# Optimization experiments

Measured on AMD Instinct MI355X. Metric: run time of the kernel, lower is better.

The kernel has to match this reference:

```python
import jax, jax.numpy as jnp
import numpy as np

B, C, H, W = 4, 64, 160, 160
OUT = 64
KS = (5, 7)


def conv2d(x, w, b=None, pad=0, groups=1):
    y = jax.lax.conv_general_dilated(
        x, w, (1, 1), [(pad, pad), (pad, pad)],
        feature_group_count=groups,
        dimension_numbers=('NCHW', 'OIHW', 'NCHW'))
    return y if b is None else y + b[None, :, None, None]


def bn_eval(x, g, b, m, v, eps=1e-5):
    s = g / jnp.sqrt(v + eps)
    return x * s[None, :, None, None] + (b - m * s)[None, :, None, None]


def boundary_attn(x, w1, b1, w2, b2):
    Cc = x.shape[1]
    kx = jnp.array([[-1., 0., 1.], [-2., 0., 2.], [-1., 0., 1.]], jnp.float32)
    ky = jnp.array([[-1., -2., -1.], [0., 0., 0.], [1., 2., 1.]], jnp.float32)
    sobel = jnp.concatenate([jnp.tile(kx[None, None], (Cc, 1, 1, 1)),
                             jnp.tile(ky[None, None], (Cc, 1, 1, 1))], axis=0)  # [2C,1,3,3]
    # grouped conv (groups=C): same output-channel grouping semantics as torch
    edge = jnp.abs(conv2d(x, sobel, pad=1, groups=Cc))
    edge = (edge[:, :Cc] + edge[:, Cc:]).mean(axis=1, keepdims=True)
    a = jax.nn.relu(conv2d(x, w1, b1, pad=1))
    a = conv2d(a, w2, b2, pad=0)
    a = jax.nn.sigmoid(a + edge)
    return x * a + x


def icc(off, half_k):
    # iterative cumulative constraint over the (small, static) K channel axis
    K = off.shape[1]
    cs = [None] * K
    cs[half_k] = off[:, half_k]
    for i in range(1, half_k + 1):
        cs[half_k - i] = 0.5 * cs[half_k - i + 1] + 0.5 * off[:, half_k - i]
        cs[half_k + i] = 0.5 * cs[half_k + i - 1] + 0.5 * off[:, half_k + i]
    c = jnp.stack(cs, axis=1)
    w = jnp.ones((K, 1, 3, 3), jnp.float32) / 9.0
    return conv2d(c, w, pad=1, groups=K)


def tumor_center(x):
    _, _, Hx, Wx = x.shape
    fs = x.mean(axis=1)  # [B,H,W]
    hg = jnp.arange(Hx, dtype=x.dtype)[None, :, None]
    wg = jnp.arange(Wx, dtype=x.dtype)[None, None, :]
    tot = fs.sum(axis=(1, 2)) + 1e-6
    return (fs * hg).sum(axis=(1, 2)) / tot, (fs * wg).sum(axis=(1, 2)) / tot


def dyn1d(x, kw, kb, K, O):
    # Original Dynamic1DConv reshapes x to [B*H*W, C, 1, 1] and grid_samples a
    # [1,K] grid per pixel. With align_corners=True a 1x1 input maps every grid
    # coordinate to ix=iy=0, so sampled[n,c,k] == x[b,c,h,w] for all k; the
    # bmm with per-pixel kernels followed by sum over C therefore collapses to
    # (sum_c x) * (sum_k kernels) -- same math, no giant gather materialized.
    Bx, _, Hx, Wx = x.shape
    ker = conv2d(x, kw, kb, pad=0).reshape(Bx, O, K, Hx, Wx)
    return x.sum(axis=1, keepdims=True) * ker.sum(axis=2)


def reference(x, ba_w1, ba_b1, ba_w2, ba_b2,
              off_w1, off_b1, off_bn_g, off_bn_b, off_bn_m, off_bn_v,
              off_w2, off_b2,
              rk5_w, rk5_b, rk7_w, rk7_b,
              lk5_w, lk5_b, lk7_w, lk7_b,
              sf_w, sf_b, sf_bn_g, sf_bn_b, sf_bn_m, sf_bn_v,
              fc_w, fc_b):
    residual = x  # in_channels == out_channels -> nn.Identity
    xa = boundary_attn(x, ba_w1, ba_b1, ba_w2, ba_b2)
    # offset branch (faithful to original; mathematically dead because the
    # per-pixel grid_sample ignores its grid -- see dyn1d). BN in eval mode.
    raw = conv2d(xa, off_w1, off_b1, pad=1)
    raw = jax.nn.relu(bn_eval(raw, off_bn_g, off_bn_b, off_bn_m, off_bn_v))
    raw = conv2d(raw, off_w2, off_b2, pad=1)
    sumk, idx = sum(KS), 0
    _offs = []
    for k in KS:
        _offs.append(icc(jnp.tanh(raw[:, idx:idx + k]), k // 2))
        _offs.append(icc(jnp.tanh(raw[:, sumk + idx:sumk + idx + k]), k // 2))
        idx += k
    _hc, _wc = tumor_center(xa)  # also dead w.r.t. output
    O = OUT // 2 // len(KS)  # 16 channels per scale per flow type
    feats = [dyn1d(xa, rk5_w, rk5_b, 5, O), dyn1d(xa, rk7_w, rk7_b, 7, O),
             dyn1d(xa, lk5_w, lk5_b, 5, O), dyn1d(xa, lk7_w, lk7_b, 7, O)]
    fusion = jnp.concatenate(feats, axis=1)  # [B, OUT, H, W]
    y = jax.nn.relu(bn_eval(conv2d(fusion, sf_w, sf_b, pad=1),
                            sf_bn_g, sf_bn_b, sf_bn_m, sf_bn_v))
    y = conv2d(y, fc_w, fc_b, pad=0)
    return y + residual


def setup_inputs() -> dict:
    key = jax.random.key(0)
    keys = iter(jax.random.split(key, 40))
    def nrm(shape, s=0.05):
        return jax.random.normal(next(keys), shape, jnp.float32) * s
    d = {}
    d['x'] = nrm((B, C, H, W), 1.0)
    d['ba_w1'] = nrm((C // 2, C, 3, 3)); d['ba_b1'] = nrm((C // 2,))
    d['ba_w2'] = nrm((1, C // 2, 1, 1)); d['ba_b2'] = nrm((1,))
    d['off_w1'] = nrm((C // 2, C, 3, 3)); d['off_b1'] = nrm((C // 2,))
    d['off_bn_g'] = 1.0 + nrm((C // 2,)); d['off_bn_b'] = nrm((C // 2,))
    d['off_bn_m'] = nrm((C // 2,))
    d['off_bn_v'] = jax.random.uniform(next(keys), (C // 2,), jnp.float32, 0.5, 1.5)
    d['off_w2'] = nrm((2 * sum(KS), C // 2, 3, 3)); d['off_b2'] = nrm((2 * sum(KS),))
    O = OUT // 2 // len(KS)
    for name, k in (('rk5', 5), ('rk7', 7), ('lk5', 5), ('lk7', 7)):
        d[name + '_w'] = nrm((O * k, C, 1, 1)); d[name + '_b'] = nrm((O * k,))
    d['sf_w'] = nrm((OUT, OUT, 3, 3)); d['sf_b'] = nrm((OUT,))
    d['sf_bn_g'] = 1.0 + nrm((OUT,)); d['sf_bn_b'] = nrm((OUT,))
    d['sf_bn_m'] = nrm((OUT,))
    d['sf_bn_v'] = jax.random.uniform(next(keys), (OUT,), jnp.float32, 0.5, 1.5)
    d['fc_w'] = nrm((OUT, OUT, 1, 1)); d['fc_b'] = nrm((OUT,))
    return d
```

## Files before the change

### kernel.cpp

```cpp
#include <hip/hip_runtime.h>
#include <hip/hip_bf16.h>
#include <math.h>

#define BB 4
#define CC 64
#define HH 160
#define WW 160
#define HWs (HH*WW)
#define NPIX (BB*HWs)

using bf16 = __hip_bfloat16;
typedef __attribute__((ext_vector_type(8)))  short short8v;
typedef __attribute__((ext_vector_type(16))) float float16v;

__device__ __forceinline__ unsigned short f2bfu(float f){
    union { bf16 h; unsigned short u; } cv; cv.h = __float2bfloat16(f); return cv.u;
}
__device__ __forceinline__ float bfu2f(unsigned short u){
    union { float f; unsigned int i; } cv; cv.i = ((unsigned int)u)<<16; return cv.f;
}
__device__ __forceinline__ float16v fzero16(){
    float16v z;
    #pragma unroll
    for(int i=0;i<16;i++) z[i]=0.f;
    return z;
}

constexpr int B1X1 = 0;
constexpr int SFBo = 64;
constexpr int SFWf = 128;
constexpr int BAWf = 18560;
constexpr int FUWf = 27776;
constexpr int FCWf = 29824;
constexpr int WS_FLOATS = 31872;

__global__ void k_prep(const float* __restrict__ rk5w, const float* __restrict__ rk5b,
                       const float* __restrict__ rk7w, const float* __restrict__ rk7b,
                       const float* __restrict__ lk5w, const float* __restrict__ lk5b,
                       const float* __restrict__ lk7w, const float* __restrict__ lk7b,
                       const float* __restrict__ sfw,  const float* __restrict__ sfb,
                       const float* __restrict__ bng,  const float* __restrict__ bnb,
                       const float* __restrict__ bnm,  const float* __restrict__ bnv,
                       const float* __restrict__ baw1, const float* __restrict__ fcw,
                       float* __restrict__ ws)
{
    int tid = blockIdx.x*blockDim.x + threadIdx.x;
    int nt  = gridDim.x*blockDim.x;
    for(int o=tid;o<64;o+=nt){
        int grp=o>>4, oo=o&15; int K=(grp&1)?7:5;
        const float* bp = (grp==0)?rk5b:(grp==1)?rk7b:(grp==2)?lk5b:lk7b;
        float s=0.f; for(int k=0;k<K;k++) s += bp[oo*K+k];
        ws[B1X1+o]=s;
    }
    for(int oc=tid;oc<64;oc+=nt){
        float sc = bng[oc]*rsqrtf(bnv[oc]+1e-5f);
        ws[SFBo+oc] = sfb[oc]*sc + bnb[oc] - bnm[oc]*sc;
    }
    unsigned short* sfwf = (unsigned short*)(ws + SFWf);
    for(int idx=tid; idx<36864; idx+=nt){
        int og = idx/18432;  int rem = idx - og*18432;
        int f  = rem>>9;     int r2 = rem & 511;
        int lane = r2>>3;    int j = r2&7;
        int tap = f>>2, kc = f&3;
        int oc = og*32 + (lane&31);
        int ic = kc*16 + (lane>>5)*8 + j;
        float sc = bng[oc]*rsqrtf(bnv[oc]+1e-5f);
        sfwf[idx] = f2bfu(sfw[(oc*64+ic)*9 + tap] * sc);
    }
    unsigned short* bawf = (unsigned short*)(ws + BAWf);
    for(int idx=tid; idx<18432; idx+=nt){
        int f  = idx>>9;     int r2 = idx & 511;
        int lane = r2>>3;    int j = r2&7;
        int tap = f>>2, kc = f&3;
        int oc = lane&31;
        int ic = kc*16 + (lane>>5)*8 + j;
        bawf[idx] = f2bfu(baw1[(oc*64+ic)*9 + tap]);
    }
    unsigned short* fuwf = (unsigned short*)(ws + FUWf);
    for(int idx=tid; idx<4096; idx+=nt){
        int og   = idx>>11;
        int kc   = (idx>>9)&3;
        int lane = (idx>>3)&63;
        int j    = idx&7;
        int oc = og*32 + (lane&31);
        int c  = kc*16 + (lane>>5)*8 + j;
        int grp = oc>>4, oo = oc&15; int K = (grp&1)?7:5;
        const float* w = (grp==0)?rk5w:(grp==1)?rk7w:(grp==2)?lk5w:lk7w;
        float s = 0.f;
        for(int k=0;k<K;k++) s += w[(oo*K+k)*64 + c];
        fuwf[idx] = f2bfu(s);
    }
    unsigned short* fcwf = (unsigned short*)(ws + FCWf);
    for(int idx=tid; idx<4096; idx+=nt){
        int og   = idx>>11;
        int kc   = (idx>>9)&3;
        int lane = (idx>>3)&63;
        int j    = idx&7;
        int oc = og*32 + (lane&31);
        int c  = kc*16 + (lane>>5)*8 + j;
        fcwf[idx] = f2bfu(fcw[oc*64 + c]);
    }
}

__global__ __launch_bounds__(256)
void k_x2nhwc(const float* __restrict__ x, unsigned short* __restrict__ xb)
{
    __shared__ unsigned short ls[128*72];
    const int t = threadIdx.x;
    const int p0 = blockIdx.x*128;
    const int b = p0 / HWs, pp0 = p0 % HWs;
    const float4* xb4 = (const float4*)(x + (size_t)b*CC*HWs + pp0);
    #pragma unroll
    for(int iter=0; iter<8; iter++){
        int idx = iter*256 + t;
        int c = idx>>5, g = idx&31;
        float4 v = xb4[(size_t)c*(HWs/4) + g];
        int px = g*4;
        int bs = (c>>3) ^ ((g>>1)&7);
        unsigned short* base = ls + bs*8 + (c&7);
        base[(px+0)*72] = f2bfu(v.x);
        base[(px+1)*72] = f2bfu(v.y);
        base[(px+2)*72] = f2bfu(v.z);
        base[(px+3)*72] = f2bfu(v.w);
    }
    __syncthreads();
    #pragma unroll
    for(int iter=0; iter<4; iter++){
        int idx = iter*256 + t;
        int sub = idx&7, px = idx>>3;
        int bs = sub ^ ((px>>3)&7);
        short8v v = *(short8v*)(ls + px*72 + bs*8);
        *(short8v*)(xb + ((size_t)(p0+px))*64 + sub*8) = v;
    }
}

__global__ __launch_bounds__(256)
void k_fuse(const unsigned short* __restrict__ xb, const float* __restrict__ bab1,
            const float* __restrict__ baw2, const float* __restrict__ bab2,
            const float* __restrict__ ws, const float* __restrict__ fcb,
            const float* __restrict__ x, float* __restrict__ out)
{
    __shared__ unsigned short xt[240*72];
    __shared__ unsigned short ftile[180*72];
    __shared__ float ebuf[2][180];
    const int bw = blockIdx.x, bh = blockIdx.y, b = blockIdx.z;
    const int t = threadIdx.x;
    const int wave = t>>6, lane = t&63;
    const int half = lane>>5, n = lane&31;
    const int w0 = bw*16, h0 = bh*8;

    const unsigned short* fb = xb + (size_t)b*HWs*64;
    for(int idx=t; idx<1920; idx+=256){
        int sub = idx&7; int pix = idx>>3;
        int r = pix/20, c = pix - r*20;
        int gh = h0-2+r, gw = w0-2+c;
        short8v v = {0,0,0,0,0,0,0,0};
        if(gh>=0&&gh<HH&&gw>=0&&gw<WW)
            v = *(const short8v*)(fb + ((size_t)(gh*WW+gw))*64 + sub*8);
        *(short8v*)(xt + pix*72 + sub*8) = v;
    }
    __syncthreads();

    float czr[2], sxr[2];
    const unsigned short* bawf = (const unsigned short*)(ws + BAWf);
    #pragma unroll
    for(int rep=0; rep<2; rep++){
        int g = wave + rep*4;
        if(g < 6){
            int p = g*32 + n; if(p > 179) p = 179;
            int pr = p/18, pc = p - pr*18;
            float16v acc = fzero16();
            #pragma unroll
            for(int kc=0; kc<4; kc++){
                short8v af[9];
                #pragma unroll
                for(int tap=0; tap<9; tap++)
                    af[tap] = *(const short8v*)(bawf + (((size_t)(tap*4+kc))*64 + lane)*8);
                #pragma unroll
                for(int tap=0; tap<9; tap++){
                    const int dh = tap/3, dw = tap%3;
                    short8v bf = *(const short8v*)(xt + ((pr+dh)*20 + pc+dw)*72
                                                   + kc*16 + half*8);
                    acc = __builtin_amdgcn_mfma_f32_32x32x16_bf16(af[tap], bf, acc, 0,0,0);
                }
            }
            float cz = 0.f;
            #pragma unroll
            for(int r=0;r<16;r++){
                int oc = (r&3) + 8*(r>>2) + 4*half;
                cz += fmaxf(acc[r]+bab1[oc],0.f)*baw2[oc];
            }
            cz += __shfl_xor(cz, 32);
            czr[rep] = cz;
            short8v ones;
            #pragma unroll
            for(int j=0;j<8;j++) ones[j] = (short)0x3F80;
            float16v s = fzero16();
            #pragma unroll
            for(int kc=0; kc<4; kc++){
                short8v bf = *(const short8v*)(xt + ((pr+1)*20 + pc+1)*72 + kc*16 + half*8);
                s = __builtin_amdgcn_mfma_f32_32x32x16_bf16(ones, bf, s, 0,0,0);
            }
            sxr[rep] = s[0];
        }
    }

    for(int idx=t; idx<360; idx+=256){
        const int hf = (idx>=180) ? 1 : 0;
        const int px2 = idx - hf*180;
        const int r = px2/18, c = px2 - (px2/18)*18;
        float e = 0.f;
        #pragma unroll
        for(int s=0; s<4; s++){
            const int sub = hf*4 + s;
            if(hf==0){
                short8v a0 = *(const short8v*)(xt + ((r  )*20 + c  )*72 + sub*8);
                short8v a2 = *(const short8v*)(xt + ((r  )*20 + c+2)*72 + sub*8);
                short8v a3 = *(const short8v*)(xt + ((r+1)*20 + c  )*72 + sub*8);
                short8v a5 = *(const short8v*)(xt + ((r+1)*20 + c+2)*72 + sub*8);
                short8v a6 = *(const short8v*)(xt + ((r+2)*20 + c  )*72 + sub*8);
                short8v a8 = *(const short8v*)(xt + ((r+2)*20 + c+2)*72 + sub*8);
                #pragma unroll
                for(int j=0;j<8;j++){
                    float gx = (bfu2f((unsigned short)a2[j]) - bfu2f((unsigned short)a0[j]))
                       + 2.f*(bfu2f((unsigned short)a5[j]) - bfu2f((unsigned short)a3[j]))
                       +      (bfu2f((unsigned short)a8[j]) - bfu2f((unsigned short)a6[j]));
                    e += fabsf(gx);
                }
            } else {
                short8v b0 = *(const short8v*)(xt + ((r  )*20 + c  )*72 + sub*8);
                short8v b1 = *(const short8v*)(xt + ((r  )*20 + c+1)*72 + sub*8);
                short8v b2 = *(const short8v*)(xt + ((r  )*20 + c+2)*72 + sub*8);
                short8v b6 = *(const short8v*)(xt + ((r+2)*20 + c  )*72 + sub*8);
                short8v b7 = *(const short8v*)(xt + ((r+2)*20 + c+1)*72 + sub*8);
                short8v b8 = *(const short8v*)(xt + ((r+2)*20 + c+2)*72 + sub*8);
                #pragma unroll
                for(int j=0;j<8;j++){
                    float gy = (bfu2f((unsigned short)b6[j]) - bfu2f((unsigned short)b0[j]))
                       + 2.f*(bfu2f((unsigned short)b7[j]) - bfu2f((unsigned short)b1[j]))
                       +      (bfu2f((unsigned short)b8[j]) - bfu2f((unsigned short)b2[j]));
                    e += fabsf(gy);
                }
            }
        }
        ebuf[hf][px2] = e;
    }
    __syncthreads();

    const unsigned short* fuwf = (const unsigned short*)(ws + FUWf);
    #pragma unroll
    for(int rep=0; rep<2; rep++){
        int g = wave + rep*4;
        if(g < 6){
            int p0g = g*32 + n;
            bool wr = (p0g < 180);
            int p = wr ? p0g : 179;
            int pr = p/18, pc = p - pr*18;
            float z = czr[rep] + bab2[0] + (ebuf[0][p] + ebuf[1][p]) * (1.f/32.f);
            float A = 1.f + 1.f/(1.f+__expf(-z));
            float Q = A * sxr[rep];
            float P = A * Q;
            #pragma unroll
            for(int og=0; og<2; og++){
                float16v a = fzero16();
                #pragma unroll
                for(int kc=0; kc<4; kc++){
                    short8v wf = *(const short8v*)(fuwf + (((size_t)og*4 + kc)*64 + lane)*8);
                    short8v bf = *(const short8v*)(xt + ((pr+1)*20 + pc+1)*72 + kc*16 + half*8);
                    a = __builtin_amdgcn_mfma_f32_32x32x16_bf16(wf, bf, a, 0,0,0);
                }
                float bq[16];
                #pragma unroll
                for(int r=0;r<16;r++) bq[r] = ws[B1X1 + og*32 + (r&3)+8*(r>>2)+4*half];
                unsigned short* base = ftile + p*72 + og*32 + 4*half;
                #pragma unroll
                for(int gq=0; gq<4; gq++){
                    union { unsigned long long u; unsigned short s[4]; } pk;
                    #pragma unroll
                    for(int rr=0; rr<4; rr++)
                        pk.s[rr] = f2bfu(P*a[4*gq+rr] + Q*bq[4*gq+rr]);
                    if(wr) *(unsigned long long*)(base + 8*gq) = pk.u;
                }
            }
        }
    }
    __syncthreads();

    const int row = 2*wave + (n>>4), col = n&15;
    const unsigned short* sfwf = (const unsigned short*)(ws + SFWf);
    const unsigned short* fcwf = (const unsigned short*)(ws + FCWf);
    float16v F0 = fzero16(), F1 = fzero16();

    #pragma unroll
    for(int og=0; og<2; og++){
        float16v Y = fzero16();
        #pragma unroll
        for(int kc=0; kc<4; kc++){
            short8v af[9];
            #pragma unroll
            for(int tap=0; tap<9; tap++)
                af[tap] = *(const short8v*)(sfwf + (((size_t)og*36 + tap*4+kc)*64 + lane)*8);
            #pragma unroll
            for(int tap=0; tap<9; tap++){
                const int dh = tap/3, dw = tap%3;
                short8v bf = *(const short8v*)(ftile + ((row+dh)*18 + col+dw)*72
                                               + kc*16 + half*8);
                Y = __builtin_amdgcn_mfma_f32_32x32x16_bf16(af[tap], bf, Y, 0,0,0);
            }
        }
        unsigned short yb[16];
        #pragma unroll
        for(int r=0;r<16;r++){
            float bias = ws[SFBo + og*32 + (r&3)+8*(r>>2)+4*half];
            yb[r] = f2bfu(fmaxf(Y[r] + bias, 0.f));
        }
        #pragma unroll
        for(int kcl=0; kcl<2; kcl++){
            const int kc_fc = 2*og + kcl;
            unsigned short l0,l1,l2,l3, s0,s1,s2,s3;
            if(half==0){ l0=yb[8*kcl+0]; l1=yb[8*kcl+1]; l2=yb[8*kcl+2]; l3=yb[8*kcl+3];
                         s0=yb[8*kcl+4]; s1=yb[8*kcl+5]; s2=yb[8*kcl+6]; s3=yb[8*kcl+7]; }
            else       { l0=yb[8*kcl+4]; l1=yb[8*kcl+5]; l2=yb[8*kcl+6]; l3=yb[8*kcl+7];
                         s0=yb[8*kcl+0]; s1=yb[8*kcl+1]; s2=yb[8*kcl+2]; s3=yb[8*kcl+3]; }
            int p0 = (int)((unsigned)s0 | ((unsigned)s1<<16));
            int p1 = (int)((unsigned)s2 | ((unsigned)s3<<16));
            int r0 = __shfl_xor(p0, 32);
            int r1 = __shfl_xor(p1, 32);
            unsigned short m0 = (unsigned short)(r0 & 0xffff);
            unsigned short m1 = (unsigned short)(((unsigned)r0) >> 16);
            unsigned short m2 = (unsigned short)(r1 & 0xffff);
            unsigned short m3 = (unsigned short)(((unsigned)r1) >> 16);
            short8v B;
            if(half==0){ B[0]=(short)l0; B[1]=(short)l1; B[2]=(short)l2; B[3]=(short)l3;
                         B[4]=(short)m0; B[5]=(short)m1; B[6]=(short)m2; B[7]=(short)m3; }
            else       { B[0]=(short)m0; B[1]=(short)m1; B[2]=(short)m2; B[3]=(short)m3;
                         B[4]=(short)l0; B[5]=(short)l1; B[6]=(short)l2; B[7]=(short)l3; }
            short8v fa0 = *(const short8v*)(fcwf + (((size_t)0*4 + kc_fc)*64 + lane)*8);
            short8v fa1 = *(const short8v*)(fcwf + (((size_t)1*4 + kc_fc)*64 + lane)*8);
            F0 = __builtin_amdgcn_mfma_f32_32x32x16_bf16(fa0, B, F0, 0,0,0);
            F1 = __builtin_amdgcn_mfma_f32_32x32x16_bf16(fa1, B, F1, 0,0,0);
        }
    }
    #pragma unroll
    for(int og=0; og<2; og++){
        #pragma unroll
        for(int r=0;r<16;r++){
            int oc = og*32 + (r&3)+8*(r>>2)+4*half;
            size_t g = ((size_t)(b*CC + oc))*HWs + (h0+row)*WW + w0 + col;
            float v = (og==0) ? F0[r] : F1[r];
            out[g] = v + fcb[oc] + x[g];
        }
    }
}

extern "C" void kernel_launch(void* const* d_in, const int* in_sizes, int n_in,
                              void* d_out, int out_size, void* d_ws, size_t ws_size,
                              hipStream_t stream)
{
    const float* x     = (const float*)d_in[0];
    const float* ba_w1 = (const float*)d_in[1];
    const float* ba_b1 = (const float*)d_in[2];
    const float* ba_w2 = (const float*)d_in[3];
    const float* ba_b2 = (const float*)d_in[4];
    const float* rk5_w = (const float*)d_in[13];
    const float* rk5_b = (const float*)d_in[14];
    const float* rk7_w = (const float*)d_in[15];
    const float* rk7_b = (const float*)d_in[16];
    const float* lk5_w = (const float*)d_in[17];
    const float* lk5_b = (const float*)d_in[18];
    const float* lk7_w = (const float*)d_in[19];
    const float* lk7_b = (const float*)d_in[20];
    const float* sf_w  = (const float*)d_in[21];
    const float* sf_b  = (const float*)d_in[22];
    const float* bng   = (const float*)d_in[23];
    const float* bnb   = (const float*)d_in[24];
    const float* bnm   = (const float*)d_in[25];
    const float* bnv   = (const float*)d_in[26];
    const float* fc_w  = (const float*)d_in[27];
    const float* fc_b  = (const float*)d_in[28];

    float* wsf = (float*)d_ws;
    unsigned short* XB  = (unsigned short*)((char*)d_ws + (size_t)WS_FLOATS*4);
    float* out = (float*)d_out;

    k_prep<<<64, 256, 0, stream>>>(rk5_w,rk5_b,rk7_w,rk7_b,lk5_w,lk5_b,lk7_w,lk7_b,
                                   sf_w,sf_b,bng,bnb,bnm,bnv, ba_w1, fc_w, wsf);
    k_x2nhwc<<<NPIX/128, 256, 0, stream>>>(x, XB);
    k_fuse<<<dim3(10,20,4), 256, 0, stream>>>(XB, ba_b1, ba_w2, ba_b2, wsf, fc_b, x, out);
}
```

Baseline: 187.3 us.

## Double k_fuse block to 512 threads and split work across eight waves

k_fuse now runs with 512 threads. The six conv-pixel groups, each handled by its own wave, run concurrently with the Sobel edge work, which is moved onto the upper threads. The 3x3 smoothing conv is split by output-channel half across wave pairs, and the second half's ReLU outputs are exchanged through reused shared memory for the final 1x1 conv. The aim is to remove the serialised per-wave repetition and raise latency hiding, at the cost of an extra barrier, shared-memory traffic, and a tighter register budget from launch_bounds(512,4). A redundant zero-weighted term was also added to the gy expression.

```diff
diff --git a/kernel.cpp b/kernel.cpp
--- a/kernel.cpp
+++ b/kernel.cpp
@@ -134,7 +134,7 @@
     }
 }
 
-__global__ __launch_bounds__(256)
+__global__ __launch_bounds__(512, 4)
 void k_fuse(const unsigned short* __restrict__ xb, const float* __restrict__ bab1,
             const float* __restrict__ baw2, const float* __restrict__ bab2,
             const float* __restrict__ ws, const float* __restrict__ fcb,
@@ -150,7 +150,7 @@
     const int w0 = bw*16, h0 = bh*8;
 
     const unsigned short* fb = xb + (size_t)b*HWs*64;
-    for(int idx=t; idx<1920; idx+=256){
+    for(int idx=t; idx<1920; idx+=512){
         int sub = idx&7; int pix = idx>>3;
         int r = pix/20, c = pix - r*20;
         int gh = h0-2+r, gw = w0-2+c;
@@ -161,162 +161,166 @@
     }
     __syncthreads();
 
-    float czr[2], sxr[2];
-    const unsigned short* bawf = (const unsigned short*)(ws + BAWf);
-    #pragma unroll
-    for(int rep=0; rep<2; rep++){
-        int g = wave + rep*4;
-        if(g < 6){
-            int p = g*32 + n; if(p > 179) p = 179;
-            int pr = p/18, pc = p - pr*18;
-            float16v acc = fzero16();
+    float cz = 0.f, sx = 0.f;
+    if(wave < 6){
+        int p = wave*32 + n; if(p > 179) p = 179;
+        int pr = p/18, pc = p - pr*18;
+        const unsigned short* bawf = (const unsigned short*)(ws + BAWf);
+        float16v acc = fzero16();
+        #pragma unroll
+        for(int kc=0; kc<4; kc++){
+            short8v af[9];
+            #pragma unroll
+            for(int tap=0; tap<9; tap++)
+                af[tap] = *(const short8v*)(bawf + (((size_t)(tap*4+kc))*64 + lane)*8);
+            #pragma unroll
+            for(int tap=0; tap<9; tap++){
+                const int dh = tap/3, dw = tap%3;
+                short8v bf = *(const short8v*)(xt + ((pr+dh)*20 + pc+dw)*72
+                                               + kc*16 + half*8);
+                acc = __builtin_amdgcn_mfma_f32_32x32x16_bf16(af[tap], bf, acc, 0,0,0);
+            }
+        }
+        #pragma unroll
+        for(int r=0;r<16;r++){
+            int oc = (r&3) + 8*(r>>2) + 4*half;
+            cz += fmaxf(acc[r]+bab1[oc],0.f)*baw2[oc];
+        }
+        cz += __shfl_xor(cz, 32);
+        short8v ones;
+        #pragma unroll
+        for(int j=0;j<8;j++) ones[j] = (short)0x3F80;
+        float16v s = fzero16();
+        #pragma unroll
+        for(int kc=0; kc<4; kc++){
+            short8v bf = *(const short8v*)(xt + ((pr+1)*20 + pc+1)*72 + kc*16 + half*8);
+            s = __builtin_amdgcn_mfma_f32_32x32x16_bf16(ones, bf, s, 0,0,0);
+        }
+        sx = s[0];
+    }
+    {
+        const int i2 = 511 - t;
+        if(i2 < 360){
+            const int hf = (i2>=180) ? 1 : 0;
+            const int px2 = i2 - hf*180;
+            const int r = px2/18, c = px2 - (px2/18)*18;
+            float e = 0.f;
+            #pragma unroll
+            for(int s=0; s<4; s++){
+                const int sub = hf*4 + s;
+                if(hf==0){
+                    short8v a0 = *(const short8v*)(xt + ((r  )*20 + c  )*72 + sub*8);
+                    short8v a2 = *(const short8v*)(xt + ((r  )*20 + c+2)*72 + sub*8);
+                    short8v a3 = *(const short8v*)(xt + ((r+1)*20 + c  )*72 + sub*8);
+                    short8v a5 = *(const short8v*)(xt + ((r+1)*20 + c+2)*72 + sub*8);
+                    short8v a6 = *(const short8v*)(xt + ((r+2)*20 + c  )*72 + sub*8);
+                    short8v a8 = *(const short8v*)(xt + ((r+2)*20 + c+2)*72 + sub*8);
+                    #pragma unroll
+                    for(int j=0;j<8;j++){
+                        float gx = (bfu2f((unsigned short)a2[j]) - bfu2f((unsigned short)a0[j]))
+                           + 2.f*(bfu2f((unsigned short)a5[j]) - bfu2f((unsigned short)a3[j]))
+                           +      (bfu2f((unsigned short)a8[j]) - bfu2f((unsigned short)a6[j]));
+                        e += fabsf(gx);
+                    }
+                } else {
+                    short8v b0 = *(const short8v*)(xt + ((r  )*20 + c  )*72 + sub*8);
+                    short8v b1 = *(const short8v*)(xt + ((r  )*20 + c+1)*72 + sub*8);
+                    short8v b2 = *(const short8v*)(xt + ((r  )*20 + c+2)*72 + sub*8);
+                    short8v b6 = *(const short8v*)(xt + ((r+2)*20 + c  )*72 + sub*8);
+                    short8v b7 = *(const short8v*)(xt + ((r+2)*20 + c+1)*72 + sub*8);
+                    short8v b8 = *(const short8v*)(xt + ((r+2)*20 + c+2)*72 + sub*8);
+                    #pragma unroll
+                    for(int j=0;j<8;j++){
+                        float gy = (bfu2f((unsigned short)b6[j]) - bfu2f((unsigned short)b0[j]))
+                           + 2.f*(bfu2f((unsigned short)b7[j]) - bfu2f((unsigned short)b1[j]))
+                           +      (bfu2f((unsigned short)b2[j]) - bfu2f((unsigned short)b2[j]))*0.f
+                           +      (bfu2f((unsigned short)b8[j]) - bfu2f((unsigned short)b2[j]));
+                        e += fabsf(gy);
+                    }
+                }
+            }
+            ebuf[hf][px2] = e;
+        }
+    }
+    __syncthreads();
+
+    if(wave < 6){
+        const unsigned short* fuwf = (const unsigned short*)(ws + FUWf);
+        int p0g = wave*32 + n;
+        bool wr = (p0g < 180);
+        int p = wr ? p0g : 179;
+        int pr = p/18, pc = p - pr*18;
+        float z = cz + bab2[0] + (ebuf[0][p] + ebuf[1][p]) * (1.f/32.f);
+        float A = 1.f + 1.f/(1.f+__expf(-z));
+        float Q = A * sx;
+        float P = A * Q;
+        #pragma unroll
+        for(int og=0; og<2; og++){
+            float16v a = fzero16();
             #pragma unroll
             for(int kc=0; kc<4; kc++){
-                short8v af[9];
+                short8v wf = *(const short8v*)(fuwf + (((size_t)og*4 + kc)*64 + lane)*8);
+                short8v bf = *(const short8v*)(xt + ((pr+1)*20 + pc+1)*72 + kc*16 + half*8);
+                a = __builtin_amdgcn_mfma_f32_32x32x16_bf16(wf, bf, a, 0,0,0);
+            }
+            float bq[16];
+            #pragma unroll
+            for(int r=0;r<16;r++) bq[r] = ws[B1X1 + og*32 + (r&3)+8*(r>>2)+4*half];
+            unsigned short* base = ftile + p*72 + og*32 + 4*half;
+            #pragma unroll
+            for(int gq=0; gq<4; gq++){
+                union { unsigned long long u; unsigned short s[4]; } pk;
                 #pragma unroll
-                for(int tap=0; tap<9; tap++)
-                    af[tap] = *(const short8v*)(bawf + (((size_t)(tap*4+kc))*64 + lane)*8);
-                #pragma unroll
-                for(int tap=0; tap<9; tap++){
-                    const int dh = tap/3, dw = tap%3;
-                    short8v bf = *(const short8v*)(xt + ((pr+dh)*20 + pc+dw)*72
-                                                   + kc*16 + half*8);
-                    acc = __builtin_amdgcn_mfma_f32_32x32x16_bf16(af[tap], bf, acc, 0,0,0);
-                }
-            }
-            float cz = 0.f;
-            #pragma unroll
-            for(int r=0;r<16;r++){
-                int oc = (r&3) + 8*(r>>2) + 4*half;
-                cz += fmaxf(acc[r]+bab1[oc],0.f)*baw2[oc];
-            }
-            cz += __shfl_xor(cz, 32);
-            czr[rep] = cz;
-            short8v ones;
-            #pragma unroll
-            for(int j=0;j<8;j++) ones[j] = (short)0x3F80;
-            float16v s = fzero16();
-            #pragma unroll
-            for(int kc=0; kc<4; kc++){
-                short8v bf = *(const short8v*)(xt + ((pr+1)*20 + pc+1)*72 + kc*16 + half*8);
-                s = __builtin_amdgcn_mfma_f32_32x32x16_bf16(ones, bf, s, 0,0,0);
-            }
-            sxr[rep] = s[0];
-        }
-    }
-
-    for(int idx=t; idx<360; idx+=256){
-        const int hf = (idx>=180) ? 1 : 0;
-        const int px2 = idx - hf*180;
-        const int r = px2/18, c = px2 - (px2/18)*18;
-        float e = 0.f;
-        #pragma unroll
-        for(int s=0; s<4; s++){
-            const int sub = hf*4 + s;
-            if(hf==0){
-                short8v a0 = *(const short8v*)(xt + ((r  )*20 + c  )*72 + sub*8);
-                short8v a2 = *(const short8v*)(xt + ((r  )*20 + c+2)*72 + sub*8);
-                short8v a3 = *(const short8v*)(xt + ((r+1)*20 + c  )*72 + sub*8);
-                short8v a5 = *(const short8v*)(xt + ((r+1)*20 + c+2)*72 + sub*8);
-                short8v a6 = *(const short8v*)(xt + ((r+2)*20 + c  )*72 + sub*8);
-                short8v a8 = *(const short8v*)(xt + ((r+2)*20 + c+2)*72 + sub*8);
-                #pragma unroll
-                for(int j=0;j<8;j++){
-                    float gx = (bfu2f((unsigned short)a2[j]) - bfu2f((unsigned short)a0[j]))
-                       + 2.f*(bfu2f((unsigned short)a5[j]) - bfu2f((unsigned short)a3[j]))
-                       +      (bfu2f((unsigned short)a8[j]) - bfu2f((unsigned short)a6[j]));
-                    e += fabsf(gx);
-                }
-            } else {
-                short8v b0 = *(const short8v*)(xt + ((r  )*20 + c  )*72 + sub*8);
-                short8v b1 = *(const short8v*)(xt + ((r  )*20 + c+1)*72 + sub*8);
-                short8v b2 = *(const short8v*)(xt + ((r  )*20 + c+2)*72 + sub*8);
-                short8v b6 = *(const short8v*)(xt + ((r+2)*20 + c  )*72 + sub*8);
-                short8v b7 = *(const short8v*)(xt + ((r+2)*20 + c+1)*72 + sub*8);
-                short8v b8 = *(const short8v*)(xt + ((r+2)*20 + c+2)*72 + sub*8);
-                #pragma unroll
-                for(int j=0;j<8;j++){
-                    float gy = (bfu2f((unsigned short)b6[j]) - bfu2f((unsigned short)b0[j]))
-                       + 2.f*(bfu2f((unsigned short)b7[j]) - bfu2f((unsigned short)b1[j]))
-                       +      (bfu2f((unsigned short)b8[j]) - bfu2f((unsigned short)b2[j]));
-                    e += fabsf(gy);
-                }
-            }
-        }
-        ebuf[hf][px2] = e;
+                for(int rr=0; rr<4; rr++)
+                    pk.s[rr] = f2bfu(P*a[4*gq+rr] + Q*bq[4*gq+rr]);
+                if(wr) *(unsigned long long*)(base + 8*gq) = pk.u;
+            }
+        }
     }
     __syncthreads();
 
-    const unsigned short* fuwf = (const unsigned short*)(ws + FUWf);
-    #pragma unroll
-    for(int rep=0; rep<2; rep++){
-        int g = wave + rep*4;
-        if(g < 6){
-            int p0g = g*32 + n;
-            bool wr = (p0g < 180);
-            int p = wr ? p0g : 179;
-            int pr = p/18, pc = p - pr*18;
-            float z = czr[rep] + bab2[0] + (ebuf[0][p] + ebuf[1][p]) * (1.f/32.f);
-            float A = 1.f + 1.f/(1.f+__expf(-z));
-            float Q = A * sxr[rep];
-            float P = A * Q;
-            #pragma unroll
-            for(int og=0; og<2; og++){
-                float16v a = fzero16();
-                #pragma unroll
-                for(int kc=0; kc<4; kc++){
-                    short8v wf = *(const short8v*)(fuwf + (((size_t)og*4 + kc)*64 + lane)*8);
-                    short8v bf = *(const short8v*)(xt + ((pr+1)*20 + pc+1)*72 + kc*16 + half*8);
-                    a = __builtin_amdgcn_mfma_f32_32x32x16_bf16(wf, bf, a, 0,0,0);
-                }
-                float bq[16];
-                #pragma unroll
-                for(int r=0;r<16;r++) bq[r] = ws[B1X1 + og*32 + (r&3)+8*(r>>2)+4*half];
-                unsigned short* base = ftile + p*72 + og*32 + 4*half;
-                #pragma unroll
-                for(int gq=0; gq<4; gq++){
-                    union { unsigned long long u; unsigned short s[4]; } pk;
-                    #pragma unroll
-                    for(int rr=0; rr<4; rr++)
-                        pk.s[rr] = f2bfu(P*a[4*gq+rr] + Q*bq[4*gq+rr]);
-                    if(wr) *(unsigned long long*)(base + 8*gq) = pk.u;
-                }
-            }
-        }
-    }
-    __syncthreads();
-
-    const int row = 2*wave + (n>>4), col = n&15;
+    const int rp  = wave & 3;
+    const int og  = wave >> 2;
+    const int row = 2*rp + (n>>4), col = n&15;
     const unsigned short* sfwf = (const unsigned short*)(ws + SFWf);
     const unsigned short* fcwf = (const unsigned short*)(ws + FCWf);
-    float16v F0 = fzero16(), F1 = fzero16();
-
+
+    float16v Y = fzero16();
     #pragma unroll
-    for(int og=0; og<2; og++){
-        float16v Y = fzero16();
-        #pragma unroll
-        for(int kc=0; kc<4; kc++){
-            short8v af[9];
-            #pragma unroll
-            for(int tap=0; tap<9; tap++)
-                af[tap] = *(const short8v*)(sfwf + (((size_t)og*36 + tap*4+kc)*64 + lane)*8);
-            #pragma unroll
-            for(int tap=0; tap<9; tap++){
-                const int dh = tap/3, dw = tap%3;
-                short8v bf = *(const short8v*)(ftile + ((row+dh)*18 + col+dw)*72
-                                               + kc*16 + half*8);
-                Y = __builtin_amdgcn_mfma_f32_32x32x16_bf16(af[tap], bf, Y, 0,0,0);
-            }
-        }
-        unsigned short yb[16];
-        #pragma unroll
-        for(int r=0;r<16;r++){
-            float bias = ws[SFBo + og*32 + (r&3)+8*(r>>2)+4*half];
-            yb[r] = f2bfu(fmaxf(Y[r] + bias, 0.f));
-        }
+    for(int kc=0; kc<4; kc++){
+        short8v af[9];
+        #pragma unroll
+        for(int tap=0; tap<9; tap++)
+            af[tap] = *(const short8v*)(sfwf + (((size_t)og*36 + tap*4+kc)*64 + lane)*8);
+        #pragma unroll
+        for(int tap=0; tap<9; tap++){
+            const int dh = tap/3, dw = tap%3;
+            short8v bf = *(const short8v*)(ftile + ((row+dh)*18 + col+dw)*72
+                                           + kc*16 + half*8);
+            Y = __builtin_amdgcn_mfma_f32_32x32x16_bf16(af[tap], bf, Y, 0,0,0);
+        }
+    }
+    unsigned short yb[16];
+    #pragma unroll
+    for(int r=0;r<16;r++){
+        float bias = ws[SFBo + og*32 + (r&3)+8*(r>>2)+4*half];
+        yb[r] = f2bfu(fmaxf(Y[r] + bias, 0.f));
+    }
+    unsigned long long* ybx64 = (unsigned long long*)xt;
+    if(og==1){
+        #pragma unroll
+        for(int q=0;q<4;q++){
+            union { unsigned long long u; unsigned short s[4]; } pk;
+            #pragma unroll
+            for(int rr=0;rr<4;rr++) pk.s[rr] = yb[4*q+rr];
+            ybx64[((size_t)rp*64 + lane)*4 + q] = pk.u;
+        }
+    }
+    __syncthreads();
+    if(og==0){
+        float16v F0 = fzero16(), F1 = fzero16();
         #pragma unroll
         for(int kcl=0; kcl<2; kcl++){
-            const int kc_fc = 2*og + kcl;
             unsigned short l0,l1,l2,l3, s0,s1,s2,s3;
             if(half==0){ l0=yb[8*kcl+0]; l1=yb[8*kcl+1]; l2=yb[8*kcl+2]; l3=yb[8*kcl+3];
                          s0=yb[8*kcl+4]; s1=yb[8*kcl+5]; s2=yb[8*kcl+6]; s3=yb[8*kcl+7]; }
@@ -335,20 +339,39 @@
                          B[4]=(short)m0; B[5]=(short)m1; B[6]=(short)m2; B[7]=(short)m3; }
             else       { B[0]=(short)m0; B[1]=(short)m1; B[2]=(short)m2; B[3]=(short)m3;
                          B[4]=(short)l0; B[5]=(short)l1; B[6]=(short)l2; B[7]=(short)l3; }
+            short8v fa0 = *(const short8v*)(fcwf + (((size_t)0*4 + kcl)*64 + lane)*8);
+            short8v fa1 = *(const short8v*)(fcwf + (((size_t)1*4 + kcl)*64 + lane)*8);
+            F0 = __builtin_amdgcn_mfma_f32_32x32x16_bf16(fa0, B, F0, 0,0,0);
+            F1 = __builtin_amdgcn_mfma_f32_32x32x16_bf16(fa1, B, F1, 0,0,0);
+        }
+        #pragma unroll
+        for(int kcl=0; kcl<2; kcl++){
+            const int kc_fc = 2 + kcl;
+            const int gsel  = 2*kcl + half;
+            const int srcA  = half ? (lane^32) : lane;
+            const int srcB  = half ? lane : (lane^32);
+            unsigned long long a03 = ybx64[((size_t)rp*64 + srcA)*4 + gsel];
+            unsigned long long a47 = ybx64[((size_t)rp*64 + srcB)*4 + gsel];
+            short8v B;
+            #pragma unroll
+            for(int j2=0;j2<4;j2++){
+                B[j2]   = (short)(unsigned short)((a03 >> (16*j2)) & 0xffff);
+                B[4+j2] = (short)(unsigned short)((a47 >> (16*j2)) & 0xffff);
+            }
             short8v fa0 = *(const short8v*)(fcwf + (((size_t)0*4 + kc_fc)*64 + lane)*8);
             short8v fa1 = *(const short8v*)(fcwf + (((size_t)1*4 + kc_fc)*64 + lane)*8);
             F0 = __builtin_amdgcn_mfma_f32_32x32x16_bf16(fa0, B, F0, 0,0,0);
             F1 = __builtin_amdgcn_mfma_f32_32x32x16_bf16(fa1, B, F1, 0,0,0);
         }
-    }
-    #pragma unroll
-    for(int og=0; og<2; og++){
-        #pragma unroll
-        for(int r=0;r<16;r++){
-            int oc = og*32 + (r&3)+8*(r>>2)+4*half;
-            size_t g = ((size_t)(b*CC + oc))*HWs + (h0+row)*WW + w0 + col;
-            float v = (og==0) ? F0[r] : F1[r];
-            out[g] = v + fcb[oc] + x[g];
+        #pragma unroll
+        for(int og2=0; og2<2; og2++){
+            #pragma unroll
+            for(int r=0;r<16;r++){
+                int oc = og2*32 + (r&3)+8*(r>>2)+4*half;
+                size_t g = ((size_t)(b*CC + oc))*HWs + (h0+row)*WW + w0 + col;
+                float v = (og2==0) ? F0[r] : F1[r];
+                out[g] = v + fcb[oc] + x[g];
+            }
         }
     }
 }
@@ -386,5 +409,5 @@
     k_prep<<<64, 256, 0, stream>>>(rk5_w,rk5_b,rk7_w,rk7_b,lk5_w,lk5_b,lk7_w,lk7_b,
                                    sf_w,sf_b,bng,bnb,bnm,bnv, ba_w1, fc_w, wsf);
     k_x2nhwc<<<NPIX/128, 256, 0, stream>>>(x, XB);
-    k_fuse<<<dim3(10,20,4), 256, 0, stream>>>(XB, ba_b1, ba_w2, ba_b2, wsf, fc_b, x, out);
-}
+    k_fuse<<<dim3(10,20,4), 512, 0, stream>>>(XB, ba_b1, ba_w2, ba_b2, wsf, fc_b, x, out);
+}
```

Result: faster. 174.0 us (-7.1%).
